# Kernel tuning notes

Measured on AMD Instinct MI355X. Metric: run time of the kernel, lower is better.

The kernel has to match this reference:

```python
import jax, jax.numpy as jnp
import numpy as np

N = 50000      # nodes
E = 800000     # edges
D_IN = 128     # input_dim
NH = 64        # nhidden (per-head channels)
H = 2          # heads
TOP_K = 512
LN_EPS = 1e-5


def _ln(x, w, b):
    mu = x.mean(-1, keepdims=True)
    var = ((x - mu) ** 2).mean(-1, keepdims=True)
    return (x - mu) * jax.lax.rsqrt(var + LN_EPS) * w + b


def _gat_conv(x, edge_index, W, a_src, a_dst, bias):
    # PyG GATConv (concat=True, negative_slope=0.2, add_self_loops=True)
    n = x.shape[0]
    loops = jnp.arange(n, dtype=edge_index.dtype)
    src = jnp.concatenate([edge_index[0], loops])
    dst = jnp.concatenate([edge_index[1], loops])
    Hh, C = a_src.shape
    xp = (x @ W).reshape(n, Hh, C)                     # [N,H,C]
    al_s = (xp * a_src).sum(-1)                        # [N,H]
    al_d = (xp * a_dst).sum(-1)                        # [N,H]
    e = jax.nn.leaky_relu(al_s[src] + al_d[dst], 0.2)  # [E+N,H]
    m = jax.ops.segment_max(e, dst, num_segments=n)
    m = jnp.where(jnp.isfinite(m), m, 0.0)
    ex = jnp.exp(e - m[dst])
    denom = jax.ops.segment_sum(ex, dst, num_segments=n) + 1e-16
    alpha = ex / denom[dst]                            # scatter-softmax over dst
    out = jax.ops.segment_sum(alpha[:, :, None] * xp[src], dst, num_segments=n)
    return out.reshape(n, Hh * C) + bias


def setup_inputs() -> dict:
    key = jax.random.key(0)
    ks = jax.random.split(key, 16)
    p = lambda k, s: jax.random.normal(k, s, jnp.float32) * 0.05
    inp = {}
    inp["x1"] = jax.random.normal(ks[0], (N, D_IN), jnp.float32)
    inp["x2"] = jax.random.normal(ks[1], (N, D_IN), jnp.float32)
    inp["edge_index1"] = jax.random.randint(ks[2], (2, E), 0, N, jnp.int32)
    inp["edge_index2"] = jax.random.randint(ks[3], (2, E), 0, N, jnp.int32)
    # conv1: D_IN -> H*NH (concat)
    inp["W1"] = p(ks[4], (D_IN, H * NH))
    inp["as1"] = p(ks[5], (H, NH)); inp["ad1"] = p(ks[6], (H, NH))
    inp["b1"] = jnp.zeros((H * NH,), jnp.float32)
    # conv2: H*NH -> H*NH
    inp["W2"] = p(ks[7], (H * NH, H * NH))
    inp["as2"] = p(ks[8], (H, NH)); inp["ad2"] = p(ks[9], (H, NH))
    inp["b2"] = jnp.zeros((H * NH,), jnp.float32)
    # MLP head
    inp["fc1_w"] = p(ks[10], (TOP_K, 2 * NH)); inp["fc1_b"] = jnp.zeros((2 * NH,), jnp.float32)
    inp["ln1_w"] = jnp.ones((2 * NH,), jnp.float32); inp["ln1_b"] = jnp.zeros((2 * NH,), jnp.float32)
    inp["fc2_w"] = p(ks[11], (2 * NH, NH)); inp["fc2_b"] = jnp.zeros((NH,), jnp.float32)
    inp["ln2_w"] = jnp.ones((NH,), jnp.float32); inp["ln2_b"] = jnp.zeros((NH,), jnp.float32)
    inp["fc3_w"] = p(ks[12], (NH, 1)); inp["fc3_b"] = jnp.zeros((1,), jnp.float32)
    return inp


def _gnn(x, ei, W1, as1, ad1, b1, W2, as2, ad2, b2):
    h = jax.nn.relu(_gat_conv(x, ei, W1, as1, ad1, b1))
    return jax.nn.relu(_gat_conv(h, ei, W2, as2, ad2, b2))


def reference(x1, x2, edge_index1, edge_index2,
              W1, as1, ad1, b1, W2, as2, ad2, b2,
              fc1_w, fc1_b, ln1_w, ln1_b, fc2_w, fc2_b, ln2_w, ln2_b, fc3_w, fc3_b):
    out1 = _gnn(x1, edge_index1, W1, as1, ad1, b1, W2, as2, ad2, b2)
    out2 = _gnn(x2, edge_index2, W1, as1, ad1, b1, W2, as2, ad2, b2)
    # nn.PairwiseDistance(p=2, eps=1e-6): ||x1 - x2 + eps||_2 per row -> [N]
    diff = out1 - out2 + 1e-6
    sim = jnp.sqrt((diff * diff).sum(-1))
    topv, _ = jax.lax.top_k(sim, TOP_K)                # [TOP_K]
    h = jax.nn.relu(_ln(topv @ fc1_w + fc1_b, ln1_w, ln1_b))
    h = jax.nn.relu(_ln(h @ fc2_w + fc2_b, ln2_w, ln2_b))
    return jax.nn.sigmoid(h @ fc3_w + fc3_b)           # [1]
```

## Files before the change

### kernel.cpp

```cpp
#include <hip/hip_runtime.h>
#include <hip/hip_bf16.h>
#include <math.h>

#define N_NODES 50000
#define N_EDGES 800000
#define TOPK 512

__device__ __forceinline__ float lrelu02(float v) { return v > 0.f ? v : 0.2f * v; }

__device__ __forceinline__ unsigned short f2bf(float f) {
    unsigned u = __float_as_uint(f);
    u += 0x7fffu + ((u >> 16) & 1u);
    return (unsigned short)(u >> 16);
}

__global__ void k_count2(const int* __restrict__ ei1, const int* __restrict__ ei2,
                         int* __restrict__ cnt1, int* __restrict__ cnt2) {
    int e = blockIdx.x * 256 + threadIdx.x;
    if (e < N_EDGES) atomicAdd(&cnt1[ei1[N_EDGES + e]], 1);
    else if (e < 2 * N_EDGES) atomicAdd(&cnt2[ei2[e]], 1);
}

__global__ __launch_bounds__(1024) void k_scan1(const int* __restrict__ cnt1, const int* __restrict__ cnt2,
                                                int* __restrict__ rp1, int* __restrict__ rp2,
                                                int* __restrict__ part1, int* __restrict__ part2) {
    __shared__ int lds[1024];
    int g = blockIdx.y;
    const int* cnt = g ? cnt2 : cnt1;
    int* rp = g ? rp2 : rp1;
    int* part = g ? part2 : part1;
    int t = threadIdx.x;
    int i = blockIdx.x * 1024 + t;
    int v = (i < N_NODES) ? cnt[i] : 0;
    lds[t] = v;
    __syncthreads();
    for (int off = 1; off < 1024; off <<= 1) {
        int add = (t >= off) ? lds[t - off] : 0;
        __syncthreads();
        lds[t] += add;
        __syncthreads();
    }
    if (i < N_NODES) rp[i] = lds[t] - v;
    if (t == 1023) part[blockIdx.x] = lds[1023];
}

__global__ __launch_bounds__(128) void k_scan2(const int* __restrict__ part1, const int* __restrict__ part2,
                                               int* __restrict__ bo1, int* __restrict__ bo2,
                                               int* __restrict__ rp1, int* __restrict__ rp2) {
    int t = threadIdx.x, g = t >> 6, lane = t & 63;
    const int* part = g ? part2 : part1;
    int* bo = g ? bo2 : bo1;
    int v = (lane < 49) ? part[lane] : 0;
    int p = v;
    for (int d = 1; d < 64; d <<= 1) { int u = __shfl_up(p, d, 64); if (lane >= d) p += u; }
    if (lane < 49) bo[lane] = p - v;
    if (lane == 0) (g ? rp2 : rp1)[N_NODES] = N_EDGES;
}

__global__ __launch_bounds__(1024) void k_scan3(int* __restrict__ rp1, int* __restrict__ rp2,
                                                const int* __restrict__ bo1, const int* __restrict__ bo2) {
    int g = blockIdx.y;
    int* rp = g ? rp2 : rp1;
    int add = (g ? bo2 : bo1)[blockIdx.x];
    int i = blockIdx.x * 1024 + threadIdx.x;
    if (i < N_NODES) rp[i] += add;
}

__global__ void k_scatter2(const int* __restrict__ ei1, const int* __restrict__ ei2,
                           const int* __restrict__ rp1, const int* __restrict__ rp2,
                           int* __restrict__ cur1, int* __restrict__ cur2,
                           int* __restrict__ ssrc1, int* __restrict__ ssrc2) {
    int e = blockIdx.x * 256 + threadIdx.x;
    if (e < N_EDGES) {
        int src = ei1[e], dst = ei1[N_EDGES + e];
        ssrc1[rp1[dst] + atomicAdd(&cur1[dst], 1)] = src;
    } else if (e < 2 * N_EDGES) {
        int ee = e - N_EDGES;
        int src = ei2[ee], dst = ei2[e];
        ssrc2[rp2[dst] + atomicAdd(&cur2[dst], 1)] = src;
    }
}

template<int IN_BF16>
__global__ __launch_bounds__(256) void k_gemm_att(
    const void* __restrict__ XA_, const void* __restrict__ XB_, const float* __restrict__ W,
    const float* __restrict__ a_src, const float* __restrict__ a_dst,
    unsigned short* __restrict__ YA, unsigned short* __restrict__ YB,
    float2* __restrict__ alsA, float2* __restrict__ aldA,
    float2* __restrict__ alsB, float2* __restrict__ aldB) {
    __shared__ __align__(16) float Xs[64][128];
    __shared__ __align__(16) float Wl[128][64];
    int t = threadIdx.x;
    int head = blockIdx.y;
    int row0 = blockIdx.x * 64;
    const void* X = blockIdx.z ? XB_ : XA_;
    unsigned short* Y = blockIdx.z ? YB : YA;
    float* als = (float*)(blockIdx.z ? alsB : alsA);
    float* ald = (float*)(blockIdx.z ? aldB : aldA);

    const float4* W4 = (const float4*)W;
    float4* Wl4 = (float4*)Wl;
    #pragma unroll
    for (int i = 0; i < 8; ++i) {
        int e = i * 256 + t;
        int k = e >> 4, cc = e & 15;
        Wl4[k * 16 + cc] = W4[k * 32 + head * 16 + cc];
    }
    float4* Xs4 = (float4*)Xs;
    if (IN_BF16) {
        const uint4* Xb = (const uint4*)X;
        #pragma unroll
        for (int i = 0; i < 4; ++i) {
            int e = i * 256 + t;
            int r = e >> 4, c8 = e & 15;
            int g = row0 + r;
            uint4 v = make_uint4(0u, 0u, 0u, 0u);
            if (g < N_NODES) v = Xb[g * 16 + c8];
            float4 f0 = make_float4(__uint_as_float(v.x << 16), __uint_as_float(v.x & 0xffff0000u),
                                    __uint_as_float(v.y << 16), __uint_as_float(v.y & 0xffff0000u));
            float4 f1 = make_float4(__uint_as_float(v.z << 16), __uint_as_float(v.z & 0xffff0000u),
                                    __uint_as_float(v.w << 16), __uint_as_float(v.w & 0xffff0000u));
            int c0 = c8 * 2, c1 = c0 + 1;
            Xs4[r * 32 + ((c0 + r + (r >> 2)) & 31)] = f0;
            Xs4[r * 32 + ((c1 + r + (r >> 2)) & 31)] = f1;
        }
    } else {
        const float4* X4 = (const float4*)X;
        #pragma unroll
        for (int i = 0; i < 8; ++i) {
            int e = i * 256 + t;
            int r = e >> 5, c = e & 31;
            int g = row0 + r;
            float4 v = make_float4(0.f, 0.f, 0.f, 0.f);
            if (g < N_NODES) v = X4[(size_t)g * 32 + c];
            int ch = (c + r + (r >> 2)) & 31;
            Xs4[r * 32 + ch] = v;
        }
    }
    __syncthreads();

    int tc = t & 15, tr = t >> 4;
    int r0 = tr * 4;
    float acc[4][4];
    #pragma unroll
    for (int r = 0; r < 4; ++r)
        #pragma unroll
        for (int c = 0; c < 4; ++c) acc[r][c] = 0.f;

    for (int k = 0; k < 128; k += 4) {
        int kc = k >> 2;
        float4 w0 = *(const float4*)&Wl[k][tc * 4];
        float4 w1 = *(const float4*)&Wl[k + 1][tc * 4];
        float4 w2 = *(const float4*)&Wl[k + 2][tc * 4];
        float4 w3 = *(const float4*)&Wl[k + 3][tc * 4];
        #pragma unroll
        for (int r = 0; r < 4; ++r) {
            int row = r0 + r;
            int ch = (kc + row + (row >> 2)) & 31;
            float4 xv = Xs4[row * 32 + ch];
            acc[r][0] += xv.x * w0.x + xv.y * w1.x + xv.z * w2.x + xv.w * w3.x;
            acc[r][1] += xv.x * w0.y + xv.y * w1.y + xv.z * w2.y + xv.w * w3.y;
            acc[r][2] += xv.x * w0.z + xv.y * w1.z + xv.z * w2.z + xv.w * w3.z;
            acc[r][3] += xv.x * w0.w + xv.y * w1.w + xv.z * w2.w + xv.w * w3.w;
        }
    }

    float s0 = a_src[head * 64 + tc * 4 + 0], s1 = a_src[head * 64 + tc * 4 + 1];
    float s2 = a_src[head * 64 + tc * 4 + 2], s3 = a_src[head * 64 + tc * 4 + 3];
    float d0 = a_dst[head * 64 + tc * 4 + 0], d1 = a_dst[head * 64 + tc * 4 + 1];
    float d2 = a_dst[head * 64 + tc * 4 + 2], d3 = a_dst[head * 64 + tc * 4 + 3];

    #pragma unroll
    for (int r = 0; r < 4; ++r) {
        int g = row0 + r0 + r;
        float ps = acc[r][0] * s0 + acc[r][1] * s1 + acc[r][2] * s2 + acc[r][3] * s3;
        float pd = acc[r][0] * d0 + acc[r][1] * d1 + acc[r][2] * d2 + acc[r][3] * d3;
        #pragma unroll
        for (int m = 1; m < 16; m <<= 1) {
            ps += __shfl_xor(ps, m, 64);
            pd += __shfl_xor(pd, m, 64);
        }
        if (g < N_NODES) {
            ushort4 pk;
            pk.x = f2bf(acc[r][0]); pk.y = f2bf(acc[r][1]);
            pk.z = f2bf(acc[r][2]); pk.w = f2bf(acc[r][3]);
            *(ushort4*)&Y[(size_t)g * 128 + head * 64 + tc * 4] = pk;
            if (tc == 0) { als[g * 2 + head] = ps; ald[g * 2 + head] = pd; }
        }
    }
}

__device__ __forceinline__ void agg4(
    const unsigned short* __restrict__ xp, const float2* __restrict__ als2,
    const float2* __restrict__ ald2, const int* __restrict__ rp,
    const int* __restrict__ ssrc, int node, int lane, float* r ) {
    const uint4* xp4 = (const uint4*)xp;
    int lg = lane & 15, grp = lane >> 4;
    float2 adv = ald2[node];
    float2 asf = als2[node];
    float ws0 = __expf(lrelu02(asf.x + adv.x));
    float ws1 = __expf(lrelu02(asf.y + adv.y));
    float a0 = 0.f, a1 = 0.f, a2 = 0.f, a3 = 0.f, a4 = 0.f, a5 = 0.f, a6 = 0.f, a7 = 0.f;
    float dp0 = 0.f, dp1 = 0.f;
    int start = rp[node], end = rp[node + 1];
    for (int j0 = start; j0 < end; j0 += 64) {
        int rem = end - j0;
        int sv = 0; float w0v = 0.f, w1v = 0.f;
        if (lane < rem) {
            sv = ssrc[j0 + lane];
            float2 a = als2[sv];
            w0v = __expf(lrelu02(a.x + adv.x));
            w1v = __expf(lrelu02(a.y + adv.y));
        }
        dp0 += w0v; dp1 += w1v;
        int len = rem < 64 ? rem : 64;
        int nit = (len + 3) >> 2;
        int i = 0;
        for (; i + 2 <= nit; i += 2) {
            int la = 4 * i + grp, lb = la + 4;
            int sa = __shfl(sv, la, 64);
            int sb = __shfl(sv, lb, 64);
            float wa0 = __shfl(w0v, la, 64), wa1 = __shfl(w1v, la, 64);
            float wb0 = __shfl(w0v, lb, 64), wb1 = __shfl(w1v, lb, 64);
            uint4 va = xp4[sa * 16 + lg];
            uint4 vb = xp4[sb * 16 + lg];
            float wa = (lg >= 8) ? wa1 : wa0;
            float wb = (lg >= 8) ? wb1 : wb0;
            a0 = fmaf(wa, __uint_as_float(va.x << 16), a0);
            a1 = fmaf(wa, __uint_as_float(va.x & 0xffff0000u), a1);
            a2 = fmaf(wa, __uint_as_float(va.y << 16), a2);
            a3 = fmaf(wa, __uint_as_float(va.y & 0xffff0000u), a3);
            a4 = fmaf(wa, __uint_as_float(va.z << 16), a4);
            a5 = fmaf(wa, __uint_as_float(va.z & 0xffff0000u), a5);
            a6 = fmaf(wa, __uint_as_float(va.w << 16), a6);
            a7 = fmaf(wa, __uint_as_float(va.w & 0xffff0000u), a7);
            a0 = fmaf(wb, __uint_as_float(vb.x << 16), a0);
            a1 = fmaf(wb, __uint_as_float(vb.x & 0xffff0000u), a1);
            a2 = fmaf(wb, __uint_as_float(vb.y << 16), a2);
            a3 = fmaf(wb, __uint_as_float(vb.y & 0xffff0000u), a3);
            a4 = fmaf(wb, __uint_as_float(vb.z << 16), a4);
            a5 = fmaf(wb, __uint_as_float(vb.z & 0xffff0000u), a5);
            a6 = fmaf(wb, __uint_as_float(vb.w << 16), a6);
            a7 = fmaf(wb, __uint_as_float(vb.w & 0xffff0000u), a7);
        }
        if (i < nit) {
            int la = 4 * i + grp;
            int sa = __shfl(sv, la, 64);
            float wa0 = __shfl(w0v, la, 64), wa1 = __shfl(w1v, la, 64);
            uint4 va = xp4[sa * 16 + lg];
            float wa = (lg >= 8) ? wa1 : wa0;
            a0 = fmaf(wa, __uint_as_float(va.x << 16), a0);
            a1 = fmaf(wa, __uint_as_float(va.x & 0xffff0000u), a1);
            a2 = fmaf(wa, __uint_as_float(va.y << 16), a2);
            a3 = fmaf(wa, __uint_as_float(va.y & 0xffff0000u), a3);
            a4 = fmaf(wa, __uint_as_float(va.z << 16), a4);
            a5 = fmaf(wa, __uint_as_float(va.z & 0xffff0000u), a5);
            a6 = fmaf(wa, __uint_as_float(va.w << 16), a6);
            a7 = fmaf(wa, __uint_as_float(va.w & 0xffff0000u), a7);
        }
    }
    #pragma unroll
    for (int m = 16; m < 64; m <<= 1) {
        a0 += __shfl_xor(a0, m, 64); a1 += __shfl_xor(a1, m, 64);
        a2 += __shfl_xor(a2, m, 64); a3 += __shfl_xor(a3, m, 64);
        a4 += __shfl_xor(a4, m, 64); a5 += __shfl_xor(a5, m, 64);
        a6 += __shfl_xor(a6, m, 64); a7 += __shfl_xor(a7, m, 64);
    }
    #pragma unroll
    for (int m = 1; m < 64; m <<= 1) {
        dp0 += __shfl_xor(dp0, m, 64);
        dp1 += __shfl_xor(dp1, m, 64);
    }
    uint4 v = xp4[node * 16 + lg];
    float wss = (lg >= 8) ? ws1 : ws0;
    a0 = fmaf(wss, __uint_as_float(v.x << 16), a0);
    a1 = fmaf(wss, __uint_as_float(v.x & 0xffff0000u), a1);
    a2 = fmaf(wss, __uint_as_float(v.y << 16), a2);
    a3 = fmaf(wss, __uint_as_float(v.y & 0xffff0000u), a3);
    a4 = fmaf(wss, __uint_as_float(v.z << 16), a4);
    a5 = fmaf(wss, __uint_as_float(v.z & 0xffff0000u), a5);
    a6 = fmaf(wss, __uint_as_float(v.w << 16), a6);
    a7 = fmaf(wss, __uint_as_float(v.w & 0xffff0000u), a7);
    float inv = 1.f / (((lg >= 8) ? dp1 + ws1 : dp0 + ws0) + 1e-16f);
    r[0] = a0 * inv; r[1] = a1 * inv; r[2] = a2 * inv; r[3] = a3 * inv;
    r[4] = a4 * inv; r[5] = a5 * inv; r[6] = a6 * inv; r[7] = a7 * inv;
}

__global__ __launch_bounds__(256) void k_agg(
    const unsigned short* __restrict__ xpA, const float2* __restrict__ alsA, const float2* __restrict__ aldA,
    const int* __restrict__ rp1, const int* __restrict__ ssrc1, unsigned short* __restrict__ outA,
    const unsigned short* __restrict__ xpB, const float2* __restrict__ alsB, const float2* __restrict__ aldB,
    const int* __restrict__ rp2, const int* __restrict__ ssrc2, unsigned short* __restrict__ outB,
    const float* __restrict__ bias) {
    int x = blockIdx.x;
    int xcd = x & 7;
    int g = xcd >> 2;
    int j = (x >> 3) * 4 + (xcd & 3);
    const unsigned short* xp = g ? xpB : xpA;
    const float2* als = g ? alsB : alsA;
    const float2* ald = g ? aldB : aldA;
    const int* rp = g ? rp2 : rp1;
    const int* ssrc = g ? ssrc2 : ssrc1;
    unsigned short* out = g ? outB : outA;
    int node = j * 4 + (threadIdx.x >> 6);
    int lane = threadIdx.x & 63;
    int lg = lane & 15;
    float r[8];
    agg4(xp, als, ald, rp, ssrc, node, lane, r);
    float4 b0 = *(const float4*)&bias[8 * lg];
    float4 b1 = *(const float4*)&bias[8 * lg + 4];
    float o0 = fmaxf(r[0] + b0.x, 0.f), o1 = fmaxf(r[1] + b0.y, 0.f);
    float o2 = fmaxf(r[2] + b0.z, 0.f), o3 = fmaxf(r[3] + b0.w, 0.f);
    float o4 = fmaxf(r[4] + b1.x, 0.f), o5 = fmaxf(r[5] + b1.y, 0.f);
    float o6 = fmaxf(r[6] + b1.z, 0.f), o7 = fmaxf(r[7] + b1.w, 0.f);
    if ((lane >> 4) == 0) {
        uint4 o;
        o.x = (unsigned)f2bf(o0) | ((unsigned)f2bf(o1) << 16);
        o.y = (unsigned)f2bf(o2) | ((unsigned)f2bf(o3) << 16);
        o.z = (unsigned)f2bf(o4) | ((unsigned)f2bf(o5) << 16);
        o.w = (unsigned)f2bf(o6) | ((unsigned)f2bf(o7) << 16);
        ((uint4*)out)[node * 16 + lg] = o;
    }
}

__global__ __launch_bounds__(256) void k_dist(
    const unsigned short* __restrict__ outA, const unsigned short* __restrict__ outB,
    float* __restrict__ sim, int* __restrict__ hist) {
    int t = threadIdx.x;
    int node = blockIdx.x * 16 + (t >> 4);
    int lg = t & 15;
    uint4 va = ((const uint4*)outA)[node * 16 + lg];
    uint4 vb = ((const uint4*)outB)[node * 16 + lg];
    float p = 0.f;
    {
        float d;
        d = __uint_as_float(va.x << 16)         - __uint_as_float(vb.x << 16)         + 1e-6f; p = fmaf(d, d, p);
        d = __uint_as_float(va.x & 0xffff0000u) - __uint_as_float(vb.x & 0xffff0000u) + 1e-6f; p = fmaf(d, d, p);
        d = __uint_as_float(va.y << 16)         - __uint_as_float(vb.y << 16)         + 1e-6f; p = fmaf(d, d, p);
        d = __uint_as_float(va.y & 0xffff0000u) - __uint_as_float(vb.y & 0xffff0000u) + 1e-6f; p = fmaf(d, d, p);
        d = __uint_as_float(va.z << 16)         - __uint_as_float(vb.z << 16)         + 1e-6f; p = fmaf(d, d, p);
        d = __uint_as_float(va.z & 0xffff0000u) - __uint_as_float(vb.z & 0xffff0000u) + 1e-6f; p = fmaf(d, d, p);
        d = __uint_as_float(va.w << 16)         - __uint_as_float(vb.w << 16)         + 1e-6f; p = fmaf(d, d, p);
        d = __uint_as_float(va.w & 0xffff0000u) - __uint_as_float(vb.w & 0xffff0000u) + 1e-6f; p = fmaf(d, d, p);
    }
    #pragma unroll
    for (int m = 1; m < 16; m <<= 1) p += __shfl_xor(p, m, 64);
    if (lg == 0) {
        float sv = sqrtf(p);
        sim[node] = sv;
        atomicAdd(&hist[__float_as_uint(sv) >> 16], 1);
    }
}

__global__ __launch_bounds__(1024) void k_select2(
    const float* __restrict__ sim, const int* __restrict__ hhi,
    int* __restrict__ hlo, int* __restrict__ state) {
    __shared__ int lds[1024];
    __shared__ int sbin, scnt;
    int t = threadIdx.x;
    int base = t * 64;
    int local = 0;
    for (int i = 0; i < 64; ++i) local += hhi[base + i];
    lds[t] = local;
    __syncthreads();
    for (int off = 1; off < 1024; off <<= 1) {
        int add = (t + off < 1024) ? lds[t + off] : 0;
        __syncthreads();
        lds[t] += add;
        __syncthreads();
    }
    int incl = lds[t];
    int above = (t < 1023) ? lds[t + 1] : 0;
    if (above < TOPK && incl >= TOPK) {
        int c = above;
        for (int b = 63; b >= 0; --b) {
            int h = hhi[base + b];
            if (c + h >= TOPK) { sbin = base + b; scnt = c; break; }
            c += h;
        }
    }
    __syncthreads();
    int hb = sbin, cA = scnt;
    for (int i = t; i < N_NODES; i += 1024) {
        unsigned key = __float_as_uint(sim[i]);
        if ((int)(key >> 16) == hb) atomicAdd(&hlo[key & 0xFFFF], 1);
    }
    __threadfence();
    __syncthreads();
    int K2 = TOPK - cA;
    local = 0;
    for (int i = 0; i < 64; ++i) local += hlo[base + i];
    lds[t] = local;
    __syncthreads();
    for (int off = 1; off < 1024; off <<= 1) {
        int add = (t + off < 1024) ? lds[t + off] : 0;
        __syncthreads();
        lds[t] += add;
        __syncthreads();
    }
    incl = lds[t];
    above = (t < 1023) ? lds[t + 1] : 0;
    if (above < K2 && incl >= K2) {
        int c = above;
        for (int b = 63; b >= 0; --b) {
            int h = hlo[base + b];
            if (c + h >= K2) {
                state[2] = (int)((((unsigned)hb) << 16) | (unsigned)(base + b));
                state[3] = cA + c;
                break;
            }
            c += h;
        }
    }
}

__global__ __launch_bounds__(512) void k_sort_mlp(
    const float* __restrict__ sim, const int* __restrict__ state,
    const float* __restrict__ fc1_w, const float* __restrict__ fc1_b,
    const float* __restrict__ ln1_w, const float* __restrict__ ln1_b,
    const float* __restrict__ fc2_w, const float* __restrict__ fc2_b,
    const float* __restrict__ ln2_w, const float* __restrict__ ln2_b,
    const float* __restrict__ fc3_w, const float* __restrict__ fc3_b,
    float* __restrict__ outp) {
    __shared__ float s[512];
    __shared__ float h1p[4][128];
    __shared__ float h1[128];
    __shared__ float h2[64];
    __shared__ float stats[2];
    __shared__ int cnt;
    int t = threadIdx.x;
    unsigned T = (unsigned)state[2];
    int nG = state[3];
    if (t == 0) cnt = 0;
    __syncthreads();
    for (int i = t; i < N_NODES; i += 512) {
        float v = sim[i];
        if (__float_as_uint(v) > T) { int p = atomicAdd(&cnt, 1); s[p] = v; }
    }
    __syncthreads();
    if (t >= nG) s[t] = __uint_as_float(T);
    __syncthreads();
    for (int k = 2; k <= 512; k <<= 1)
        for (int j = k >> 1; j > 0; j >>= 1) {
            int ixj = t ^ j;
            if (ixj > t) {
                float a = s[t], b = s[ixj];
                bool up = ((t & k) == 0);
                if ((a > b) == up) { s[t] = b; s[ixj] = a; }
            }
            __syncthreads();
        }
    {
        int o = t & 127, seg = t >> 7;
        float acc = 0.f;
        for (int i = seg * 128; i < seg * 128 + 128; ++i)
            acc += s[511 - i] * fc1_w[i * 128 + o];
        h1p[seg][o] = acc;
    }
    __syncthreads();
    if (t < 128) h1[t] = fc1_b[t] + h1p[0][t] + h1p[1][t] + h1p[2][t] + h1p[3][t];
    __syncthreads();
    if (t == 0) {
        float mu = 0.f;
        for (int i = 0; i < 128; ++i) mu += h1[i];
        mu *= (1.f / 128.f);
        float var = 0.f;
        for (int i = 0; i < 128; ++i) { float d = h1[i] - mu; var += d * d; }
        var *= (1.f / 128.f);
        stats[0] = mu; stats[1] = rsqrtf(var + 1e-5f);
    }
    __syncthreads();
    if (t < 128) h1[t] = fmaxf((h1[t] - stats[0]) * stats[1] * ln1_w[t] + ln1_b[t], 0.f);
    __syncthreads();
    if (t < 64) {
        float acc = fc2_b[t];
        for (int i = 0; i < 128; ++i) acc += h1[i] * fc2_w[i * 64 + t];
        h2[t] = acc;
    }
    __syncthreads();
    if (t == 0) {
        float mu = 0.f;
        for (int i = 0; i < 64; ++i) mu += h2[i];
        mu *= (1.f / 64.f);
        float var = 0.f;
        for (int i = 0; i < 64; ++i) { float d = h2[i] - mu; var += d * d; }
        var *= (1.f / 64.f);
        stats[0] = mu; stats[1] = rsqrtf(var + 1e-5f);
    }
    __syncthreads();
    if (t < 64) h2[t] = fmaxf((h2[t] - stats[0]) * stats[1] * ln2_w[t] + ln2_b[t], 0.f);
    __syncthreads();
    if (t == 0) {
        float z = fc3_b[0];
        for (int i = 0; i < 64; ++i) z += h2[i] * fc3_w[i];
        outp[0] = 1.f / (1.f + expf(-z));
    }
}

extern "C" void kernel_launch(void* const* d_in, const int* in_sizes, int n_in,
                              void* d_out, int out_size, void* d_ws, size_t ws_size,
                              hipStream_t stream) {
    const float* x1 = (const float*)d_in[0];
    const float* x2 = (const float*)d_in[1];
    const int* ei1 = (const int*)d_in[2];
    const int* ei2 = (const int*)d_in[3];
    const float* W1 = (const float*)d_in[4];
    const float* as1 = (const float*)d_in[5];
    const float* ad1 = (const float*)d_in[6];
    const float* b1 = (const float*)d_in[7];
    const float* W2 = (const float*)d_in[8];
    const float* as2 = (const float*)d_in[9];
    const float* ad2 = (const float*)d_in[10];
    const float* b2 = (const float*)d_in[11];
    const float* fc1_w = (const float*)d_in[12];
    const float* fc1_b = (const float*)d_in[13];
    const float* ln1_w = (const float*)d_in[14];
    const float* ln1_b = (const float*)d_in[15];
    const float* fc2_w = (const float*)d_in[16];
    const float* fc2_b = (const float*)d_in[17];
    const float* ln2_w = (const float*)d_in[18];
    const float* ln2_b = (const float*)d_in[19];
    const float* fc3_w = (const float*)d_in[20];
    const float* fc3_b = (const float*)d_in[21];
    float* outp = (float*)d_out;

    char* ws = (char*)d_ws;
    size_t off = 0;
    auto alloc = [&](size_t bytes) -> void* {
        void* p = ws + off;
        off = (off + bytes + 255) & ~(size_t)255;
        return p;
    };
    unsigned short* xpA = (unsigned short*)alloc((size_t)N_NODES * 128 * 2);
    unsigned short* xpB = (unsigned short*)alloc((size_t)N_NODES * 128 * 2);
    unsigned short* tmpA = (unsigned short*)alloc((size_t)N_NODES * 128 * 2);
    unsigned short* tmpB = (unsigned short*)alloc((size_t)N_NODES * 128 * 2);
    int* ssrc1  = (int*)alloc((size_t)N_EDGES * 4);
    int* ssrc2  = (int*)alloc((size_t)N_EDGES * 4);
    int* rp1    = (int*)alloc((size_t)(N_NODES + 1) * 4);
    int* rp2    = (int*)alloc((size_t)(N_NODES + 1) * 4);
    float2* alsA = (float2*)alloc((size_t)N_NODES * 8);
    float2* aldA = (float2*)alloc((size_t)N_NODES * 8);
    float2* alsB = (float2*)alloc((size_t)N_NODES * 8);
    float2* aldB = (float2*)alloc((size_t)N_NODES * 8);
    int* part1 = (int*)alloc(64 * 4);
    int* part2 = (int*)alloc(64 * 4);
    int* bo1   = (int*)alloc(64 * 4);
    int* bo2   = (int*)alloc(64 * 4);
    float* sim = (float*)alloc((size_t)N_NODES * 4);
    char* zbase = ws + off;
    int* cnt1 = (int*)alloc((size_t)N_NODES * 4);
    int* cnt2 = (int*)alloc((size_t)N_NODES * 4);
    int* cur1 = (int*)alloc((size_t)N_NODES * 4);
    int* cur2 = (int*)alloc((size_t)N_NODES * 4);
    int* hist1 = (int*)alloc(65536 * 4);
    int* hist2 = (int*)alloc(65536 * 4);
    int* state = (int*)alloc(64);
    size_t zsize = (size_t)((ws + off) - zbase);
    hipMemsetAsync(zbase, 0, zsize, stream);

    k_count2<<<6250, 256, 0, stream>>>(ei1, ei2, cnt1, cnt2);
    k_scan1<<<dim3(49, 2), 1024, 0, stream>>>(cnt1, cnt2, rp1, rp2, part1, part2);
    k_scan2<<<1, 128, 0, stream>>>(part1, part2, bo1, bo2, rp1, rp2);
    k_scan3<<<dim3(49, 2), 1024, 0, stream>>>(rp1, rp2, bo1, bo2);
    k_scatter2<<<6250, 256, 0, stream>>>(ei1, ei2, rp1, rp2, cur1, cur2, ssrc1, ssrc2);

    dim3 ggrid(782, 2, 2);
    k_gemm_att<0><<<ggrid, 256, 0, stream>>>(x1, x2, W1, as1, ad1, xpA, xpB, alsA, aldA, alsB, aldB);
    k_agg<<<25000, 256, 0, stream>>>(xpA, alsA, aldA, rp1, ssrc1, tmpA,
                                     xpB, alsB, aldB, rp2, ssrc2, tmpB, b1);
    k_gemm_att<1><<<ggrid, 256, 0, stream>>>(tmpA, tmpB, W2, as2, ad2,
                                             xpA, xpB, alsA, aldA, alsB, aldB);
    k_agg<<<25000, 256, 0, stream>>>(xpA, alsA, aldA, rp1, ssrc1, tmpA,
                                     xpB, alsB, aldB, rp2, ssrc2, tmpB, b2);
    k_dist<<<3125, 256, 0, stream>>>(tmpA, tmpB, sim, hist1);

    k_select2<<<1, 1024, 0, stream>>>(sim, hist1, hist2, state);
    k_sort_mlp<<<1, 512, 0, stream>>>(sim, state, fc1_w, fc1_b, ln1_w, ln1_b,
                                      fc2_w, fc2_b, ln2_w, ln2_b, fc3_w, fc3_b, outp);
}
```

Baseline: 810.2 us.

## Replace histogram radix-select with sample-based threshold and bitonic top-k

```diff
diff --git a/kernel.cpp b/kernel.cpp
--- a/kernel.cpp
+++ b/kernel.cpp
@@ -325,7 +325,7 @@
 
 __global__ __launch_bounds__(256) void k_dist(
     const unsigned short* __restrict__ outA, const unsigned short* __restrict__ outB,
-    float* __restrict__ sim, int* __restrict__ hist) {
+    float* __restrict__ sim) {
     int t = threadIdx.x;
     int node = blockIdx.x * 16 + (t >> 4);
     int lg = t & 15;
@@ -345,120 +345,74 @@
     }
     #pragma unroll
     for (int m = 1; m < 16; m <<= 1) p += __shfl_xor(p, m, 64);
-    if (lg == 0) {
-        float sv = sqrtf(p);
-        sim[node] = sv;
-        atomicAdd(&hist[__float_as_uint(sv) >> 16], 1);
-    }
-}
-
-__global__ __launch_bounds__(1024) void k_select2(
-    const float* __restrict__ sim, const int* __restrict__ hhi,
-    int* __restrict__ hlo, int* __restrict__ state) {
-    __shared__ int lds[1024];
-    __shared__ int sbin, scnt;
-    int t = threadIdx.x;
-    int base = t * 64;
-    int local = 0;
-    for (int i = 0; i < 64; ++i) local += hhi[base + i];
-    lds[t] = local;
-    __syncthreads();
-    for (int off = 1; off < 1024; off <<= 1) {
-        int add = (t + off < 1024) ? lds[t + off] : 0;
-        __syncthreads();
-        lds[t] += add;
-        __syncthreads();
-    }
-    int incl = lds[t];
-    int above = (t < 1023) ? lds[t + 1] : 0;
-    if (above < TOPK && incl >= TOPK) {
-        int c = above;
-        for (int b = 63; b >= 0; --b) {
-            int h = hhi[base + b];
-            if (c + h >= TOPK) { sbin = base + b; scnt = c; break; }
-            c += h;
-        }
-    }
-    __syncthreads();
-    int hb = sbin, cA = scnt;
-    for (int i = t; i < N_NODES; i += 1024) {
-        unsigned key = __float_as_uint(sim[i]);
-        if ((int)(key >> 16) == hb) atomicAdd(&hlo[key & 0xFFFF], 1);
-    }
-    __threadfence();
-    __syncthreads();
-    int K2 = TOPK - cA;
-    local = 0;
-    for (int i = 0; i < 64; ++i) local += hlo[base + i];
-    lds[t] = local;
-    __syncthreads();
-    for (int off = 1; off < 1024; off <<= 1) {
-        int add = (t + off < 1024) ? lds[t + off] : 0;
-        __syncthreads();
-        lds[t] += add;
-        __syncthreads();
-    }
-    incl = lds[t];
-    above = (t < 1023) ? lds[t + 1] : 0;
-    if (above < K2 && incl >= K2) {
-        int c = above;
-        for (int b = 63; b >= 0; --b) {
-            int h = hlo[base + b];
-            if (c + h >= K2) {
-                state[2] = (int)((((unsigned)hb) << 16) | (unsigned)(base + b));
-                state[3] = cA + c;
-                break;
-            }
-            c += h;
-        }
-    }
-}
-
-__global__ __launch_bounds__(512) void k_sort_mlp(
-    const float* __restrict__ sim, const int* __restrict__ state,
+    if (lg == 0) sim[node] = sqrtf(p);
+}
+
+__global__ __launch_bounds__(1024) void k_topk_mlp(
+    const float* __restrict__ sim,
     const float* __restrict__ fc1_w, const float* __restrict__ fc1_b,
     const float* __restrict__ ln1_w, const float* __restrict__ ln1_b,
     const float* __restrict__ fc2_w, const float* __restrict__ fc2_b,
     const float* __restrict__ ln2_w, const float* __restrict__ ln2_b,
     const float* __restrict__ fc3_w, const float* __restrict__ fc3_b,
     float* __restrict__ outp) {
-    __shared__ float s[512];
-    __shared__ float h1p[4][128];
+    __shared__ float buf[4096];
+    __shared__ float h1p[8][128];
     __shared__ float h1[128];
     __shared__ float h2[64];
     __shared__ float stats[2];
     __shared__ int cnt;
     int t = threadIdx.x;
-    unsigned T = (unsigned)state[2];
-    int nG = state[3];
+    for (int i = t; i < 4096; i += 1024)
+        buf[i] = (i < 3125) ? sim[i * 16] : -1.0f;
+    __syncthreads();
+    for (int k = 2; k <= 4096; k <<= 1)
+        for (int j = k >> 1; j > 0; j >>= 1) {
+            for (int i = t; i < 4096; i += 1024) {
+                int ixj = i ^ j;
+                if (ixj > i) {
+                    float a = buf[i], b = buf[ixj];
+                    bool dn = ((i & k) == 0);
+                    if ((a < b) == dn) { buf[i] = b; buf[ixj] = a; }
+                }
+            }
+            __syncthreads();
+        }
+    float T = buf[127];
+    __syncthreads();
     if (t == 0) cnt = 0;
     __syncthreads();
-    for (int i = t; i < N_NODES; i += 512) {
+    for (int i = t; i < N_NODES; i += 1024) {
         float v = sim[i];
-        if (__float_as_uint(v) > T) { int p = atomicAdd(&cnt, 1); s[p] = v; }
-    }
-    __syncthreads();
-    if (t >= nG) s[t] = __uint_as_float(T);
-    __syncthreads();
-    for (int k = 2; k <= 512; k <<= 1)
+        if (v > T) { int p = atomicAdd(&cnt, 1); if (p < 4096) buf[p] = v; }
+    }
+    __syncthreads();
+    int n = cnt < 4096 ? cnt : 4096;
+    for (int i = t; i < 4096; i += 1024)
+        if (i >= n) buf[i] = -1.0f;
+    __syncthreads();
+    for (int k = 2; k <= 4096; k <<= 1)
         for (int j = k >> 1; j > 0; j >>= 1) {
-            int ixj = t ^ j;
-            if (ixj > t) {
-                float a = s[t], b = s[ixj];
-                bool up = ((t & k) == 0);
-                if ((a > b) == up) { s[t] = b; s[ixj] = a; }
+            for (int i = t; i < 4096; i += 1024) {
+                int ixj = i ^ j;
+                if (ixj > i) {
+                    float a = buf[i], b = buf[ixj];
+                    bool dn = ((i & k) == 0);
+                    if ((a < b) == dn) { buf[i] = b; buf[ixj] = a; }
+                }
             }
             __syncthreads();
         }
     {
         int o = t & 127, seg = t >> 7;
         float acc = 0.f;
-        for (int i = seg * 128; i < seg * 128 + 128; ++i)
-            acc += s[511 - i] * fc1_w[i * 128 + o];
+        for (int i = seg * 64; i < seg * 64 + 64; ++i)
+            acc += buf[i] * fc1_w[i * 128 + o];
         h1p[seg][o] = acc;
     }
     __syncthreads();
-    if (t < 128) h1[t] = fc1_b[t] + h1p[0][t] + h1p[1][t] + h1p[2][t] + h1p[3][t];
+    if (t < 128) h1[t] = fc1_b[t] + h1p[0][t] + h1p[1][t] + h1p[2][t] + h1p[3][t]
+                       + h1p[4][t] + h1p[5][t] + h1p[6][t] + h1p[7][t];
     __syncthreads();
     if (t == 0) {
         float mu = 0.f;
@@ -553,9 +507,6 @@
     int* cnt2 = (int*)alloc((size_t)N_NODES * 4);
     int* cur1 = (int*)alloc((size_t)N_NODES * 4);
     int* cur2 = (int*)alloc((size_t)N_NODES * 4);
-    int* hist1 = (int*)alloc(65536 * 4);
-    int* hist2 = (int*)alloc(65536 * 4);
-    int* state = (int*)alloc(64);
     size_t zsize = (size_t)((ws + off) - zbase);
     hipMemsetAsync(zbase, 0, zsize, stream);
 
@@ -573,9 +524,8 @@
                                              xpA, xpB, alsA, aldA, alsB, aldB);
     k_agg<<<25000, 256, 0, stream>>>(xpA, alsA, aldA, rp1, ssrc1, tmpA,
                                      xpB, alsB, aldB, rp2, ssrc2, tmpB, b2);
-    k_dist<<<3125, 256, 0, stream>>>(tmpA, tmpB, sim, hist1);
-
-    k_select2<<<1, 1024, 0, stream>>>(sim, hist1, hist2, state);
-    k_sort_mlp<<<1, 512, 0, stream>>>(sim, state, fc1_w, fc1_b, ln1_w, ln1_b,
-                                      fc2_w, fc2_b, ln2_w, ln2_b, fc3_w, fc3_b, outp);
-}
+    k_dist<<<3125, 256, 0, stream>>>(tmpA, tmpB, sim);
+
+    k_topk_mlp<<<1, 1024, 0, stream>>>(sim, fc1_w, fc1_b, ln1_w, ln1_b,
+                                       fc2_w, fc2_b, ln2_w, ln2_b, fc3_w, fc3_b, outp);
+}
```

After: 650.8 us. -19.7%, faster.
